# Kernel tuning notes

Measured on AMD Instinct MI355X. Metric: run time of the kernel, lower is better.

## Reference

```python
import jax, jax.numpy as jnp
import numpy as np

WEIGHT = 1e-7
SIGMA_RGB = 15.0
SIGMA_XY = 100.0
SCALE = 0.5


def _nearest_resize(x, Ho, Wo):
    # torch F.interpolate mode='nearest': src = floor(dst * in/out)
    H, W = x.shape[-2], x.shape[-1]
    iy = (jnp.arange(Ho) * (H / Ho)).astype(jnp.int32)
    ix = (jnp.arange(Wo) * (W / Wo)).astype(jnp.int32)
    return x[..., iy[:, None], ix[None, :]]


def _bilinear_resize(x, Ho, Wo):
    # torch bilinear, align_corners=False (half-pixel centers, no antialias)
    H, W = x.shape[-2], x.shape[-1]
    yc = jnp.clip((jnp.arange(Ho, dtype=jnp.float32) + 0.5) * (H / Ho) - 0.5, 0.0, H - 1.0)
    xc = jnp.clip((jnp.arange(Wo, dtype=jnp.float32) + 0.5) * (W / Wo) - 0.5, 0.0, W - 1.0)
    y0 = jnp.floor(yc).astype(jnp.int32); y1 = jnp.minimum(y0 + 1, H - 1); ty = yc - y0
    x0 = jnp.floor(xc).astype(jnp.int32); x1 = jnp.minimum(x0 + 1, W - 1); tx = xc - x0
    g = lambda yi, xi: x[..., yi[:, None], xi[None, :]]
    top = g(y0, x0) * (1.0 - tx) + g(y0, x1) * tx
    bot = g(y1, x0) * (1.0 - tx) + g(y1, x1) * tx
    return top * (1.0 - ty[:, None]) + bot * ty[:, None]


def _dense_energy(images, segmentations, ROIs, seg_label):
    N, K, H, W = segmentations.shape
    Ho, Wo = int(H * SCALE), int(W * SCALE)
    P = Ho * Wo
    img_s = _nearest_resize(images, Ho, Wo)            # [N,3,Ho,Wo]
    seg_s = _bilinear_resize(segmentations, Ho, Wo)    # [N,K,Ho,Wo]
    roi_s = _nearest_resize(ROIs, Ho, Wo)              # [N,Ho,Wo]
    lbl_s = _nearest_resize(seg_label, Ho, Wo)         # [N,1,Ho,Wo]
    unlabel = (lbl_s == 255)[:, 0]                     # [N,Ho,Wo]

    # Gate = clamp(ROI - max_k seg, min=0), with unlabeled region forced to 1
    gate = roi_s - jnp.max(seg_s, axis=1)
    gate = jnp.where(unlabel, 1.0, gate)
    gate = jnp.maximum(gate, 0.0)
    gate = jax.lax.stop_gradient(gate)                 # constant in the custom backward

    seg_roi = seg_s * roi_s[:, None]                   # [N,K,Ho,Wo]

    sxy = SIGMA_XY * SCALE
    yy, xx = jnp.meshgrid(jnp.arange(Ho, dtype=jnp.float32),
                          jnp.arange(Wo, dtype=jnp.float32), indexing='ij')
    pos = jnp.stack([xx.ravel() / sxy, yy.ravel() / sxy], axis=-1)  # [P,2]

    def per_image(img, seg):
        # img [3,Ho,Wo], seg [K,Ho,Wo] -> AS [K,P]: Gaussian bilateral filter
        col = img.reshape(img.shape[0], P).T / SIGMA_RGB            # [P,3]
        f = jnp.concatenate([pos, col], axis=-1)                    # [P,5]
        sq = jnp.sum(f * f, axis=-1)
        d2 = jnp.maximum(sq[:, None] + sq[None, :] - 2.0 * (f @ f.T), 0.0)
        Wm = jnp.exp(-0.5 * d2)                                     # [P,P] affinity
        return seg.reshape(seg.shape[0], P) @ Wm                    # symmetric Wm

    AS = jax.vmap(per_image)(img_s, seg_roi)                        # [N,K,P]
    AS = AS * gate.reshape(N, 1, P)
    loss = -jnp.sum(seg_roi.reshape(N, K, P) * AS) / N
    return (WEIGHT * loss).reshape(1)


def setup_inputs() -> dict:
    key = jax.random.key(0)
    k1, k2, k3, k4 = jax.random.split(key, 4)
    N, C, K, H, W = 4, 3, 21, 128, 128
    images = jax.random.uniform(k1, (N, C, H, W), dtype=jnp.float32) * 255.0
    segmentations = jax.nn.softmax(jax.random.normal(k2, (N, K, H, W), dtype=jnp.float32), axis=1)
    ROIs = jax.random.randint(k3, (N, H, W), 0, 2).astype(jnp.float32)
    seg_label = jax.random.randint(k4, (N, 1, H, W), 0, 256).astype(jnp.int32)
    return {"images": images, "segmentations": segmentations, "ROIs": ROIs, "seg_label": seg_label}


def reference(images, segmentations, ROIs, seg_label):
    return _dense_energy(images, segmentations, ROIs, seg_label)
```

## Files before the change

kernel.cpp:

```cpp
#include <hip/hip_runtime.h>
#include <hip/hip_bf16.h>


typedef _Float16 v8h __attribute__((ext_vector_type(8)));
typedef float v16f __attribute__((ext_vector_type(16)));

#define NIMG 4
#define KCH 21
#define HIN 128
#define WIN 128
#define PPX 4096
#define TPB 32
#define TRI 528
#define NBLK (NIMG * TRI)

#define WS_S_OFF 0x000000
#define WS_F_OFF 0x180000
#define PART_OFF 0x200000

#define LOG2E 1.44269504088896341f

__device__ __forceinline__ float fexp2(float x) {
#if __has_builtin(__builtin_amdgcn_exp2f)
    return __builtin_amdgcn_exp2f(x);
#else
    return __expf(x * 0.69314718055994531f);
#endif
}

__global__ __launch_bounds__(256) void prep_kernel(
    const float* __restrict__ img, const float* __restrict__ seg,
    const float* __restrict__ roi, const int* __restrict__ lbl,
    char* __restrict__ ws)
{
    int gid = blockIdx.x * 256 + threadIdx.x;
    int n = gid >> 12, p = gid & (PPX - 1);
    int y = p >> 6, x = p & 63, iy = 2 * y, ix = 2 * x;
    const float inv_rgb = 1.0f / 15.0f, inv_sxy = 1.0f / 50.0f;

    float rv = roi[((size_t)n * HIN + iy) * WIN + ix];
    int   lb = lbl[((size_t)n * HIN + iy) * WIN + ix];

    float sv[KCH]; float maxs = 0.0f;
    #pragma unroll
    for (int k = 0; k < KCH; k++) {
        const float* sp = seg + ((((size_t)n * KCH + k) * HIN + iy) * WIN + ix);
        float2 a = *(const float2*)sp;
        float2 c = *(const float2*)(sp + WIN);
        float s = 0.25f * (a.x + a.y + c.x + c.y);
        maxs = fmaxf(maxs, s);
        sv[k] = s * rv;
    }
    float gate = (lb == 255) ? 1.0f : fmaxf(rv - maxs, 0.0f);

    union { float4 q[6]; _Float16 e[48]; } rs;
    #pragma unroll
    for (int k = 0; k < KCH; k++) {
        rs.e[k] = (_Float16)(sv[k] * gate);
        rs.e[24 + k] = (_Float16)sv[k];
    }
    #pragma unroll
    for (int k = KCH; k < 24; k++) { rs.e[k] = (_Float16)0.f; rs.e[24 + k] = (_Float16)0.f; }

    float f[5];
    f[0] = (float)x * inv_sxy;
    f[1] = (float)y * inv_sxy;
    f[2] = img[(((size_t)n * 3 + 0) * HIN + iy) * WIN + ix] * inv_rgb;
    f[3] = img[(((size_t)n * 3 + 1) * HIN + iy) * WIN + ix] * inv_rgb;
    f[4] = img[(((size_t)n * 3 + 2) * HIN + iy) * WIN + ix] * inv_rgb;

    _Float16 hi[5], lo[5];
    float sq = 0.f;
    #pragma unroll
    for (int u = 0; u < 5; u++) {
        hi[u] = (_Float16)f[u];
        lo[u] = (_Float16)(f[u] - (float)hi[u]);
        float fe = (float)hi[u] + (float)lo[u];
        sq = fmaf(fe, fe, sq);
    }
    float sqv = -0.5f * sq;
    _Float16 sqh = (_Float16)sqv;
    _Float16 sql = (_Float16)(sqv - (float)sqh);
    const _Float16 h0 = (_Float16)0.f, h1 = (_Float16)1.f;

    union { float4 q[2]; _Float16 e[16]; } rf;
    #pragma unroll
    for (int u = 0; u < 5; u++) { rf.e[u] = hi[u]; rf.e[8 + u] = lo[u]; }
    rf.e[5] = sqh; rf.e[6] = sql; rf.e[7] = h1;
    rf.e[13] = h0; rf.e[14] = h0; rf.e[15] = h1;

    float4* ds = (float4*)(ws + WS_S_OFF + (size_t)gid * 96);
    #pragma unroll
    for (int u = 0; u < 6; u++) ds[u] = rs.q[u];
    float4* df = (float4*)(ws + WS_F_OFF + (size_t)gid * 32);
    df[0] = rf.q[0]; df[1] = rf.q[1];
}

#define LSTR 104
#define FSTR 40
#define SREG_O 0
#define FREG_O 26624
#define RED_O  36864
#define LDS_BYTES 36880

__global__ __launch_bounds__(256)
__attribute__((amdgpu_waves_per_eu(1, 4)))
void pairs_kernel(
    const char* __restrict__ ws, float* __restrict__ part)
{
    __shared__ __align__(16) char smem[LDS_BYTES];
    int b = blockIdx.x;
    int n = b / TRI, r = b - n * TRI;
    int i = 0, rowlen = TPB;
    while (r >= rowlen) { r -= rowlen; rowlen--; i++; }
    int j = i + r;
    bool diag = (i == j);

    int t = threadIdx.x;
    int lane = t & 63, half = lane >> 5, lr = lane & 31, wv = t >> 6;
    int wq = wv & 1, wp = wv >> 1;

    {
        const float4* gsi = (const float4*)(ws + WS_S_OFF) + (size_t)(n * PPX + i * 128) * 6;
        #pragma unroll
        for (int k = 0; k < 3; k++) {
            int v = t + k * 256;
            int row = v / 6, off = v - row * 6;
            float4 vs = gsi[v];
            char* dS = smem + SREG_O + row * LSTR + off * 16;
            *(float2*)dS = make_float2(vs.x, vs.y);
            *(float2*)(dS + 8) = make_float2(vs.z, vs.w);
        }
        const float4* gfi = (const float4*)(ws + WS_F_OFF) + (size_t)(n * PPX + i * 128) * 2;
        {
            int row = t >> 1, off = t & 1;
            float4 vf = gfi[t];
            char* dF = smem + FREG_O + row * FSTR + off * 16;
            *(float2*)dF = make_float2(vf.x, vf.y);
            *(float2*)(dF + 8) = make_float2(vf.z, vf.w);
        }
        if (!diag) {
            const float4* gsj = (const float4*)(ws + WS_S_OFF) + (size_t)(n * PPX + j * 128) * 6;
            #pragma unroll
            for (int k = 0; k < 3; k++) {
                int v = t + k * 256;
                int row = v / 6, off = v - row * 6;
                float4 vs = gsj[v];
                char* dS = smem + SREG_O + (128 + row) * LSTR + off * 16;
                *(float2*)dS = make_float2(vs.x, vs.y);
                *(float2*)(dS + 8) = make_float2(vs.z, vs.w);
            }
            const float4* gfj = (const float4*)(ws + WS_F_OFF) + (size_t)(n * PPX + j * 128) * 2;
            int row = t >> 1, off = t & 1;
            float4 vf = gfj[t];
            char* dF = smem + FREG_O + (128 + row) * FSTR + off * 16;
            *(float2*)dF = make_float2(vf.x, vf.y);
            *(float2*)(dF + 8) = make_float2(vf.z, vf.w);
        }
    }
    __syncthreads();

    int jrow0 = diag ? 0 : 128;
    const _Float16 selA = half ? (_Float16)0.f : (_Float16)1.f;
    float ac0 = 0.f, ac1 = 0.f, ac2 = 0.f, ac3 = 0.f;

    #pragma unroll
    for (int sp = 0; sp < 2; sp++) {
        int pr = wp * 64 + sp * 32 + lr;
        const char* sb = smem + SREG_O + pr * LSTR;
        const char* fb = smem + FREG_O + pr * FSTR;
        union { v8h h; float2 f[2]; } A0, A1, A2, Af;
        A0.f[0] = *(const float2*)(sb + half * 16);
        A0.f[1] = *(const float2*)(sb + half * 16 + 8);
        A1.f[0] = *(const float2*)(sb + 32 + half * 16);
        A1.f[1] = *(const float2*)(sb + 32 + half * 16 + 8);
        A2.f[0] = *(const float2*)(sb + 64 + half * 16);
        A2.f[1] = *(const float2*)(sb + 64 + half * 16 + 8);
        Af.f[0] = *(const float2*)(fb + half * 16);
        Af.f[1] = *(const float2*)(fb + half * 16 + 8);

        #pragma unroll
        for (int s = 0; s < 2; s++) {
            int cr = jrow0 + wq * 64 + s * 32 + lr;
            const char* cb = smem + SREG_O + cr * LSTR;
            const char* gb = smem + FREG_O + cr * FSTR;
            union { v8h h; float2 f[2]; } B0, B1, B2;
            union { v8h h; float2 f[2]; _Float16 e[8]; } U, L;
            B0.f[0] = *(const float2*)(cb + 48 + half * 16);
            B0.f[1] = *(const float2*)(cb + 48 + half * 16 + 8);
            int o1 = half ? 0 : 80;
            B1.f[0] = *(const float2*)(cb + o1);
            B1.f[1] = *(const float2*)(cb + o1 + 8);
            B2.f[0] = *(const float2*)(cb + 16 + half * 16);
            B2.f[1] = *(const float2*)(cb + 16 + half * 16 + 8);
            U.f[0] = *(const float2*)(gb);      U.f[1] = *(const float2*)(gb + 8);
            L.f[0] = *(const float2*)(gb + 16); L.f[1] = *(const float2*)(gb + 24);

            union { v8h h; _Float16 e[8]; } Bf1, Bf2;
            Bf1.h = U.h;
            Bf1.e[5] = selA; Bf1.e[6] = selA;
            Bf1.e[7] = half ? U.e[6] : U.e[5];
            Bf2.h = L.h;
            Bf2.e[7] = (_Float16)0.f;

            v16f z = {0.f,0.f,0.f,0.f,0.f,0.f,0.f,0.f,0.f,0.f,0.f,0.f,0.f,0.f,0.f,0.f};
            v16f c2 = __builtin_amdgcn_mfma_f32_32x32x16_f16(Af.h, Bf1.h, z, 0, 0, 0);
            c2 = __builtin_amdgcn_mfma_f32_32x32x16_f16(Af.h, Bf2.h, c2, 0, 0, 0);
            v16f c1 = __builtin_amdgcn_mfma_f32_32x32x16_f16(A0.h, B0.h, z, 0, 0, 0);
            c1 = __builtin_amdgcn_mfma_f32_32x32x16_f16(A1.h, B1.h, c1, 0, 0, 0);
            c1 = __builtin_amdgcn_mfma_f32_32x32x16_f16(A2.h, B2.h, c1, 0, 0, 0);

            #pragma unroll
            for (int rr = 0; rr < 16; rr++) {
                float arg = fminf(LOG2E * c2[rr], 0.0f);
                float w = fexp2(arg);
                if ((rr & 3) == 0)      ac0 = fmaf(w, c1[rr], ac0);
                else if ((rr & 3) == 1) ac1 = fmaf(w, c1[rr], ac1);
                else if ((rr & 3) == 2) ac2 = fmaf(w, c1[rr], ac2);
                else                    ac3 = fmaf(w, c1[rr], ac3);
            }
        }
    }

    float acc = (ac0 + ac1) + (ac2 + ac3);
    #pragma unroll
    for (int off = 32; off > 0; off >>= 1) acc += __shfl_down(acc, off, 64);
    float* wred = (float*)(smem + RED_O);
    if ((t & 63) == 0) wred[t >> 6] = acc;
    __syncthreads();
    if (t == 0) {
        float partial = (wred[0] + wred[1]) + (wred[2] + wred[3]);
        if (diag) partial *= 0.5f;
        part[b] = partial;
    }
}

__global__ __launch_bounds__(256) void finalize_kernel(
    const float* __restrict__ part, float* __restrict__ out)
{
    __shared__ float s[256];
    int t = threadIdx.x;
    float v = 0.f;
    #pragma unroll
    for (int k = 0; k < 9; k++) {
        int idx = t + k * 256;
        if (idx < NBLK) v += part[idx];
    }
    s[t] = v;
    __syncthreads();
    #pragma unroll
    for (int off = 128; off > 0; off >>= 1) {
        if (t < off) s[t] += s[t + off];
        __syncthreads();
    }
    if (t == 0) out[0] = s[0] * (-1e-7f / (float)NIMG);
}

extern "C" void kernel_launch(void* const* d_in, const int* in_sizes, int n_in,
                              void* d_out, int out_size, void* d_ws, size_t ws_size,
                              hipStream_t stream) {
    const float* images = (const float*)d_in[0];
    const float* seg    = (const float*)d_in[1];
    const float* rois   = (const float*)d_in[2];
    const int*   lbl    = (const int*)d_in[3];
    float* out = (float*)d_out;
    char*  ws  = (char*)d_ws;
    float* part = (float*)(ws + PART_OFF);

    hipLaunchKernelGGL(prep_kernel, dim3((NIMG * PPX) / 256), dim3(256), 0, stream,
                       images, seg, rois, lbl, ws);
    hipLaunchKernelGGL(pairs_kernel, dim3(NBLK), dim3(256), 0, stream,
                       (const char*)ws, part);
    hipLaunchKernelGGL(finalize_kernel, dim3(1), dim3(256), 0, stream,
                       (const float*)part, out);
}
```

Measured before the change: 82.24 us.

## Compact ROI-active pixels and skip pair tiles beyond active count

Adds a scan kernel that prefix-sums nonzero ROI pixels per image and writes a compacted destination index, so prep stores only ROI-active pixels contiguously and the pairs kernel exits early for tiles past the active count. Pixels with zero ROI contribute nothing because seg_roi is zero there, so about half the pixel pairs are skipped with random binary ROIs. It also folds log2(e) into the feature scaling so the exp argument no longer needs a multiply. The cost is an extra small launch and a data-dependent tile count. Load imbalance remains, since the early-exit blocks are still launched.

```diff
diff --git a/kernel.cpp b/kernel.cpp
--- a/kernel.cpp
+++ b/kernel.cpp
@@ -17,8 +17,10 @@
 #define WS_S_OFF 0x000000
 #define WS_F_OFF 0x180000
 #define PART_OFF 0x200000
-
-#define LOG2E 1.44269504088896341f
+#define CNT_OFF  0x202100
+#define DEST_OFF 0x202200
+
+#define SQRT_LOG2E 1.2011224087864498f
 
 __device__ __forceinline__ float fexp2(float x) {
 #if __has_builtin(__builtin_amdgcn_exp2f)
@@ -26,6 +28,58 @@
 #else
     return __expf(x * 0.69314718055994531f);
 #endif
+}
+
+__global__ __launch_bounds__(256) void scan_kernel(
+    const float* __restrict__ roi, char* __restrict__ ws)
+{
+    int n = blockIdx.x, t = threadIdx.x;
+    int y  = t >> 2;
+    int x0 = (t & 3) * 16;
+    const float* row = roi + ((size_t)n * HIN + 2 * y) * WIN + 2 * x0;
+
+    unsigned flags = 0; int cl = 0;
+    #pragma unroll
+    for (int v = 0; v < 8; v++) {
+        float4 q = *(const float4*)(row + 4 * v);
+        if (q.x != 0.f) { flags |= 1u << (2 * v);     cl++; }
+        if (q.z != 0.f) { flags |= 1u << (2 * v + 1); cl++; }
+    }
+
+    int lane = t & 63, wv = t >> 6;
+    int v = cl;
+    #pragma unroll
+    for (int off = 1; off < 64; off <<= 1) {
+        int u = __shfl_up(v, off, 64);
+        if (lane >= off) v += u;
+    }
+    __shared__ int wsum[4];
+    if (lane == 63) wsum[wv] = v;
+    __syncthreads();
+    int base = 0;
+    #pragma unroll
+    for (int k = 0; k < 4; k++) if (k < wv) base += wsum[k];
+    int excl  = base + v - cl;
+    int total = wsum[0] + wsum[1] + wsum[2] + wsum[3];
+
+    unsigned short* dest = (unsigned short*)(ws + DEST_OFF) + (size_t)n * PPX;
+    int p0 = t * 16;
+    #pragma unroll
+    for (int u = 0; u < 16; u++) {
+        if (flags & (1u << u)) dest[p0 + u] = (unsigned short)(excl++);
+    }
+    if (t == 0) ((int*)(ws + CNT_OFF))[n] = total;
+
+    int padEnd = (total + 127) & ~127;
+    if (padEnd > PPX) padEnd = PPX;
+    const float4 z4 = make_float4(0.f, 0.f, 0.f, 0.f);
+    for (int s = total + t; s < padEnd; s += 256) {
+        float4* dS = (float4*)(ws + WS_S_OFF + ((size_t)n * PPX + s) * 96);
+        #pragma unroll
+        for (int u = 0; u < 6; u++) dS[u] = z4;
+        float4* dF = (float4*)(ws + WS_F_OFF + ((size_t)n * PPX + s) * 32);
+        dF[0] = z4; dF[1] = z4;
+    }
 }
 
 __global__ __launch_bounds__(256) void prep_kernel(
@@ -36,10 +90,14 @@
     int gid = blockIdx.x * 256 + threadIdx.x;
     int n = gid >> 12, p = gid & (PPX - 1);
     int y = p >> 6, x = p & 63, iy = 2 * y, ix = 2 * x;
-    const float inv_rgb = 1.0f / 15.0f, inv_sxy = 1.0f / 50.0f;
+    const float inv_rgb = SQRT_LOG2E / 15.0f, inv_sxy = SQRT_LOG2E / 50.0f;
 
     float rv = roi[((size_t)n * HIN + iy) * WIN + ix];
-    int   lb = lbl[((size_t)n * HIN + iy) * WIN + ix];
+    if (rv == 0.0f) return;
+    int d = ((const unsigned short*)(ws + DEST_OFF))[gid];
+    int slot = (n << 12) | d;
+
+    int lb = lbl[((size_t)n * HIN + iy) * WIN + ix];
 
     float sv[KCH]; float maxs = 0.0f;
     #pragma unroll
@@ -89,10 +147,10 @@
     rf.e[5] = sqh; rf.e[6] = sql; rf.e[7] = h1;
     rf.e[13] = h0; rf.e[14] = h0; rf.e[15] = h1;
 
-    float4* ds = (float4*)(ws + WS_S_OFF + (size_t)gid * 96);
+    float4* ds = (float4*)(ws + WS_S_OFF + (size_t)slot * 96);
     #pragma unroll
     for (int u = 0; u < 6; u++) ds[u] = rs.q[u];
-    float4* df = (float4*)(ws + WS_F_OFF + (size_t)gid * 32);
+    float4* df = (float4*)(ws + WS_F_OFF + (size_t)slot * 32);
     df[0] = rf.q[0]; df[1] = rf.q[1];
 }
 
@@ -115,6 +173,13 @@
     while (r >= rowlen) { r -= rowlen; rowlen--; i++; }
     int j = i + r;
     bool diag = (i == j);
+
+    int cnt = ((const int*)(ws + CNT_OFF))[n];
+    int Tn = (cnt + 127) >> 7;
+    if (j >= Tn) {
+        if (threadIdx.x == 0) part[b] = 0.f;
+        return;
+    }
 
     int t = threadIdx.x;
     int lane = t & 63, half = lane >> 5, lr = lane & 31, wv = t >> 6;
@@ -212,7 +277,7 @@
 
             #pragma unroll
             for (int rr = 0; rr < 16; rr++) {
-                float arg = fminf(LOG2E * c2[rr], 0.0f);
+                float arg = fminf(c2[rr], 0.0f);
                 float w = fexp2(arg);
                 if ((rr & 3) == 0)      ac0 = fmaf(w, c1[rr], ac0);
                 else if ((rr & 3) == 1) ac1 = fmaf(w, c1[rr], ac1);
@@ -267,6 +332,8 @@
     char*  ws  = (char*)d_ws;
     float* part = (float*)(ws + PART_OFF);
 
+    hipLaunchKernelGGL(scan_kernel, dim3(NIMG), dim3(256), 0, stream,
+                       rois, ws);
     hipLaunchKernelGGL(prep_kernel, dim3((NIMG * PPX) / 256), dim3(256), 0, stream,
                        images, seg, rois, lbl, ws);
     hipLaunchKernelGGL(pairs_kernel, dim3(NBLK), dim3(256), 0, stream,
```

Result: faster. 79.29 us (-3.6%).
